# Kernel tuning notes

Measured on AMD Instinct MI355X. Metric: run time of the kernel, lower is better.

The kernel has to match this reference:

```python
import jax, jax.numpy as jnp
import numpy as np

H, W = 16, 16
DIM = 512
HEADS = 8
DIM_HEAD = 64
INNER = HEADS * DIM_HEAD  # 512
B = 8
N = H * W  # 256
SCALE = DIM_HEAD ** -0.5
EPS = 1e-5


def _index_map(h, w):
    # index_map[n, m] = dx * (2w-1) + dy with dx = x-i+h-1, dy = y-j+w-1
    xs = np.arange(h)
    ys = np.arange(w)
    dx = xs[:, None] - xs[None, :] + h - 1            # (h, h)
    dy = ys[:, None] - ys[None, :] + w - 1            # (w, w)
    idx = dx[:, None, :, None] * (2 * w - 1) + dy[None, :, None, :]  # (h, w, h, w)
    return idx.reshape(h * w, h * w).astype(np.int32)


def setup_inputs() -> dict:
    key = jax.random.key(0)
    ks = jax.random.split(key, 5)
    x = jax.random.normal(ks[0], (B, N, DIM), dtype=jnp.float32)
    ln_g = jnp.ones((DIM,), jnp.float32)
    ln_b = jnp.zeros((DIM,), jnp.float32)
    w_qkv = jax.random.normal(ks[1], (DIM, 3 * INNER), jnp.float32) * 0.02
    unique_params = jax.random.normal(ks[2], ((2 * H - 1) * (2 * W - 1), INNER), jnp.float32) * 0.02
    w_out = jax.random.normal(ks[3], (INNER, DIM), jnp.float32) * 0.02
    b_out = jnp.zeros((DIM,), jnp.float32)
    idx_map = jnp.asarray(_index_map(H, W))  # (N, N) int32
    return {"x": x, "ln_g": ln_g, "ln_b": ln_b, "w_qkv": w_qkv,
            "unique_params": unique_params, "w_out": w_out, "b_out": b_out,
            "idx_map": idx_map}


def reference(x, ln_g, ln_b, w_qkv, unique_params, w_out, b_out, idx_map):
    b, n, _ = x.shape
    # LayerNorm
    mu = jnp.mean(x, axis=-1, keepdims=True)
    var = jnp.mean(jnp.square(x - mu), axis=-1, keepdims=True)
    xn = (x - mu) * jax.lax.rsqrt(var + EPS) * ln_g + ln_b
    # qkv projection (no bias)
    qkv = xn @ w_qkv                                  # (b, n, 3*inner)
    q, k, v = jnp.split(qkv, 3, axis=-1)
    q = q.reshape(b, n, HEADS, DIM_HEAD)
    k = k.reshape(b, n, HEADS, DIM_HEAD)
    v = v.reshape(b, n, HEADS, DIM_HEAD)
    # attention scores
    dots = jnp.einsum('bnhd,bmhd->bhnm', q, k) * SCALE
    attn = jax.nn.softmax(dots, axis=-1)              # (b, h, n, m)
    # relative-position table: (n, m, h, d)
    rpos = unique_params[idx_map].reshape(n, n, HEADS, DIM_HEAD)
    # out[b,h,n,d] = sum_m attn[b,h,n,m] * (v[b,m,h,d] + rpos[n,m,h,d])
    out = jnp.einsum('bhnm,bmhd->bnhd', attn, v) \
        + jnp.einsum('bhnm,nmhd->bnhd', attn, rpos)
    out = out.reshape(b, n, INNER)
    return out @ w_out + b_out
```

## Files before the change

### kernel.cpp

```cpp
#include <hip/hip_runtime.h>
#include <math.h>

#define NB 8
#define SEQ 256
#define DIMC 512
#define NHEAD 8
#define DHEAD 64
#define SCALEF 0.125f

typedef __attribute__((ext_vector_type(8))) short s16x8;
typedef __attribute__((ext_vector_type(4))) float f32x4;

typedef __attribute__((address_space(3))) unsigned int lds_u32_t;
typedef const __attribute__((address_space(1))) unsigned int g_u32_t;
static __device__ __forceinline__ void gl_lds16(const void* gsrc, void* ldst) {
  __builtin_amdgcn_global_load_lds((g_u32_t*)gsrc, (lds_u32_t*)ldst, 16, 0, 0);
}

static __device__ __forceinline__ unsigned short f2bf(float f) {
  union { float f; unsigned u; } c; c.f = f;
  unsigned r = c.u + 0x7FFF + ((c.u >> 16) & 1);
  return (unsigned short)(r >> 16);
}
static __device__ __forceinline__ float bf2f(unsigned short u) {
  union { unsigned u; float f; } c; c.u = ((unsigned)u) << 16;
  return c.f;
}

static __device__ void tcast_body(const float* __restrict__ W,
    unsigned short* __restrict__ WT, int K, int N, int n0, int k0, int t,
    float (*tile)[65]) {
#pragma unroll
  for (int i = 0; i < 16; ++i) {
    const int idx = i * 256 + t;
    const int kl = idx >> 6, nl = idx & 63;
    tile[kl][nl] = W[(size_t)(k0 + kl) * N + n0 + nl];
  }
  __syncthreads();
#pragma unroll
  for (int i = 0; i < 16; ++i) {
    const int idx = i * 256 + t;
    const int nl = idx >> 6, kl = idx & 63;
    WT[(size_t)(n0 + nl) * K + k0 + kl] = f2bf(tile[kl][nl]);
  }
}

__global__ __launch_bounds__(256) void prep_kernel(const float* __restrict__ x,
    const float* __restrict__ g, const float* __restrict__ bta,
    const float* __restrict__ w_qkv, const float* __restrict__ w_out,
    const float* __restrict__ up, unsigned short* __restrict__ xnb,
    unsigned short* __restrict__ wqt, unsigned short* __restrict__ wot,
    unsigned short* __restrict__ upb) {
  __shared__ float tile[64][65];
  __shared__ float sh_s[4], sh_q[4];
  const int t = threadIdx.x;
  const int bid = blockIdx.x;
  if (bid < 192) {
    tcast_body(w_qkv, wqt, 512, 1536, (bid % 24) * 64, (bid / 24) * 64, t, tile);
  } else if (bid < 256) {
    const int b2 = bid - 192;
    tcast_body(w_out, wot, 512, 512, (b2 % 8) * 64, (b2 / 8) * 64, t, tile);
  } else if (bid < 497) {
    const int base = (bid - 256) * 2048 + t * 4;
#pragma unroll
    for (int it = 0; it < 2; ++it) {
      const int i = base + it * 1024;
      if (i < 492032) {
        const float4 v = *(const float4*)&up[i];
        ushort4 w;
        w.x = f2bf(v.x); w.y = f2bf(v.y); w.z = f2bf(v.z); w.w = f2bf(v.w);
        *(ushort4*)&upb[i] = w;
      }
    }
  } else {
    const int row = bid - 497;
    const float2 v = ((const float2*)(x + (size_t)row * DIMC))[t];
    float s = v.x + v.y;
    float q = v.x * v.x + v.y * v.y;
#pragma unroll
    for (int off = 32; off > 0; off >>= 1) {
      s += __shfl_down(s, off);
      q += __shfl_down(q, off);
    }
    const int wave = t >> 6, lane = t & 63;
    if (lane == 0) { sh_s[wave] = s; sh_q[wave] = q; }
    __syncthreads();
    const float fs = sh_s[0] + sh_s[1] + sh_s[2] + sh_s[3];
    const float fq = sh_q[0] + sh_q[1] + sh_q[2] + sh_q[3];
    const float mean = fs * (1.0f / DIMC);
    const float inv = rsqrtf(fq * (1.0f / DIMC) - mean * mean + 1e-5f);
    const float2 gv = ((const float2*)g)[t];
    const float2 bv = ((const float2*)bta)[t];
    ushort2 o;
    o.x = f2bf((v.x - mean) * inv * gv.x + bv.x);
    o.y = f2bf((v.y - mean) * inv * gv.y + bv.y);
    ((ushort2*)(xnb + (size_t)row * DIMC))[t] = o;
  }
}

template <int BM, int BN, bool BIAS, bool OUTBF, bool VSPLIT>
__global__ __launch_bounds__(256) void mfma_gemm_bt(
    const unsigned short* __restrict__ A, const unsigned short* __restrict__ BT,
    const float* __restrict__ bias, void* __restrict__ Cv,
    unsigned short* __restrict__ vtb, int M, int K, int N) {
  constexpr int TR = BM / 32;
  constexpr int TC = BN / 32;
  __shared__ unsigned short As[BM * 32];
  __shared__ unsigned short Bs[BN * 32];
  const int t = threadIdx.x;
  const int wave = t >> 6, lane = t & 63;
  const int wr = wave >> 1, wc = wave & 1;
  const int bm = blockIdx.x * BM, bn = blockIdx.y * BN;

  f32x4 acc[TR][TC] = {};

  const int fr = lane & 15, q4 = lane >> 4;
  const int kBlocks = K >> 5;
  for (int kb = 0; kb < kBlocks; ++kb) {
    const int k0 = kb << 5;
    __syncthreads();
#pragma unroll
    for (int c = 0; c < (BM * 4 + 255) / 256; ++c) {
      const int p = c * 256 + t;
      if (BM * 4 % 256 == 0 || p < BM * 4) {
        const int row = p >> 2;
        const int jl = (p & 3) ^ ((row >> 1) & 3);
        gl_lds16(A + (size_t)(bm + row) * K + k0 + jl * 8,
                 As + (size_t)(c * 256 + wave * 64) * 8);
      }
    }
#pragma unroll
    for (int c = 0; c < (BN * 4 + 255) / 256; ++c) {
      const int p = c * 256 + t;
      if (BN * 4 % 256 == 0 || p < BN * 4) {
        const int row = p >> 2;
        const int jl = (p & 3) ^ ((row >> 1) & 3);
        gl_lds16(BT + (size_t)(bn + row) * K + k0 + jl * 8,
                 Bs + (size_t)(c * 256 + wave * 64) * 8);
      }
    }
    __syncthreads();
    s16x8 af[TR], bfr[TC];
#pragma unroll
    for (int i = 0; i < TR; ++i) {
      const int row = wr * (BM / 2) + i * 16 + fr;
      const int jp = q4 ^ ((row >> 1) & 3);
      af[i] = *(const s16x8*)(As + row * 32 + jp * 8);
    }
#pragma unroll
    for (int j = 0; j < TC; ++j) {
      const int row = wc * (BN / 2) + j * 16 + fr;
      const int jp = q4 ^ ((row >> 1) & 3);
      bfr[j] = *(const s16x8*)(Bs + row * 32 + jp * 8);
    }
#pragma unroll
    for (int i = 0; i < TR; ++i)
#pragma unroll
      for (int j = 0; j < TC; ++j)
        acc[i][j] = __builtin_amdgcn_mfma_f32_16x16x32_bf16(af[i], bfr[j],
                                                            acc[i][j], 0, 0, 0);
  }
  if (VSPLIT && bn >= 1024) {
#pragma unroll
    for (int i = 0; i < TR; ++i) {
#pragma unroll
      for (int j = 0; j < TC; ++j) {
        const int hc = bn - 1024 + wc * (BN / 2) + j * 16 + fr;
        const int h = hc >> 6, d = hc & 63;
#pragma unroll
        for (int r = 0; r < 4; ++r) {
          const int row = bm + wr * (BM / 2) + i * 16 + q4 * 4 + r;
          const int b = row >> 8, m = row & 255;
          vtb[(size_t)((b * 8 + h) * 64 + d) * 256 + m] = f2bf(acc[i][j][r]);
        }
      }
    }
    return;
  }
#pragma unroll
  for (int i = 0; i < TR; ++i) {
#pragma unroll
    for (int j = 0; j < TC; ++j) {
      const int col = bn + wc * (BN / 2) + j * 16 + fr;
      const float bv = BIAS ? bias[col] : 0.0f;
#pragma unroll
      for (int r = 0; r < 4; ++r) {
        const int row = bm + wr * (BM / 2) + i * 16 + q4 * 4 + r;
        if constexpr (OUTBF) {
          ((unsigned short*)Cv)[(size_t)row * N + col] = f2bf(acc[i][j][r] + bv);
        } else {
          ((float*)Cv)[(size_t)row * N + col] = acc[i][j][r] + bv;
        }
      }
    }
  }
}

#define PSTR 264
#define KSTR 72
__global__ __launch_bounds__(128) void fused_attn_kernel(
    const unsigned short* __restrict__ qkvb, const unsigned short* __restrict__ vtb,
    unsigned short* __restrict__ attnb, unsigned short* __restrict__ oav) {
  __shared__ unsigned short kv_lds[256 * KSTR];
  __shared__ unsigned short p_lds[32 * PSTR];
  const int bh = blockIdx.y, b = bh >> 3, h = bh & 7;
  const int n0 = blockIdx.x * 32;
  const int t = threadIdx.x, wave = t >> 6, lane = t & 63;
  const int fr = lane & 15, q4 = lane >> 4;

#pragma unroll
  for (int p = 0; p < 16; ++p) {
    const int chunk = p * 128 + t;
    const int m = chunk >> 3, c = chunk & 7;
    *(s16x8*)(kv_lds + m * KSTR + c * 8) =
        *(const s16x8*)(qkvb + (size_t)(b * SEQ + m) * 1536 + 512 + h * 64 + c * 8);
  }
  s16x8 qf[2];
  {
    const size_t qrow = (size_t)(b * SEQ + n0 + wave * 16 + fr) * 1536 + h * 64;
#pragma unroll
    for (int ks = 0; ks < 2; ++ks)
      qf[ks] = *(const s16x8*)(qkvb + qrow + ks * 32 + q4 * 8);
  }
  __syncthreads();

  f32x4 s[16];
#pragma unroll
  for (int mt = 0; mt < 16; ++mt) s[mt] = (f32x4){0.f, 0.f, 0.f, 0.f};
#pragma unroll
  for (int ks = 0; ks < 2; ++ks)
#pragma unroll
    for (int mt = 0; mt < 16; ++mt) {
      const s16x8 kf =
          *(const s16x8*)(kv_lds + (mt * 16 + fr) * KSTR + ks * 32 + q4 * 8);
      s[mt] = __builtin_amdgcn_mfma_f32_16x16x32_bf16(qf[ks], kf, s[mt], 0, 0, 0);
    }

  float mx[4] = {-1e30f, -1e30f, -1e30f, -1e30f};
#pragma unroll
  for (int mt = 0; mt < 16; ++mt)
#pragma unroll
    for (int r = 0; r < 4; ++r) {
      s[mt][r] *= SCALEF;
      mx[r] = fmaxf(mx[r], s[mt][r]);
    }
#pragma unroll
  for (int r = 0; r < 4; ++r) {
    mx[r] = fmaxf(mx[r], __shfl_xor(mx[r], 1));
    mx[r] = fmaxf(mx[r], __shfl_xor(mx[r], 2));
    mx[r] = fmaxf(mx[r], __shfl_xor(mx[r], 4));
    mx[r] = fmaxf(mx[r], __shfl_xor(mx[r], 8));
  }
  float sum[4] = {0.f, 0.f, 0.f, 0.f};
#pragma unroll
  for (int mt = 0; mt < 16; ++mt)
#pragma unroll
    for (int r = 0; r < 4; ++r) {
      s[mt][r] = __expf(s[mt][r] - mx[r]);
      sum[r] += s[mt][r];
    }
#pragma unroll
  for (int r = 0; r < 4; ++r) {
    sum[r] += __shfl_xor(sum[r], 1);
    sum[r] += __shfl_xor(sum[r], 2);
    sum[r] += __shfl_xor(sum[r], 4);
    sum[r] += __shfl_xor(sum[r], 8);
  }
  const float invs[4] = {1.0f / sum[0], 1.0f / sum[1], 1.0f / sum[2],
                         1.0f / sum[3]};

  __syncthreads();

  {
    const int nb = wave * 16 + q4 * 4;
#pragma unroll
    for (int mt = 0; mt < 16; ++mt)
#pragma unroll
      for (int r = 0; r < 4; ++r)
        p_lds[(nb + r) * PSTR + mt * 16 + fr] = f2bf(s[mt][r] * invs[r]);
  }
#pragma unroll
  for (int p = 0; p < 16; ++p) {
    const int idx = p * 128 + t;
    const int d = idx >> 5, c = idx & 31;
    *(s16x8*)(kv_lds + d * PSTR + c * 8) =
        *(const s16x8*)(vtb + (size_t)(bh * 64 + d) * 256 + c * 8);
  }
  __syncthreads();

#pragma unroll
  for (int p = 0; p < 8; ++p) {
    const int idx = p * 128 + t;
    const int row = idx >> 5, mc = (idx & 31) * 8;
    *(s16x8*)(attnb + (size_t)(bh * SEQ + n0 + row) * SEQ + mc) =
        *(const s16x8*)(p_lds + row * PSTR + mc);
  }

  f32x4 o[4];
#pragma unroll
  for (int dt = 0; dt < 4; ++dt) o[dt] = (f32x4){0.f, 0.f, 0.f, 0.f};
#pragma unroll
  for (int ks = 0; ks < 8; ++ks) {
    const s16x8 pf =
        *(const s16x8*)(p_lds + (wave * 16 + fr) * PSTR + ks * 32 + q4 * 8);
#pragma unroll
    for (int dt = 0; dt < 4; ++dt) {
      const s16x8 vf =
          *(const s16x8*)(kv_lds + (dt * 16 + fr) * PSTR + ks * 32 + q4 * 8);
      o[dt] = __builtin_amdgcn_mfma_f32_16x16x32_bf16(pf, vf, o[dt], 0, 0, 0);
    }
  }
#pragma unroll
  for (int dt = 0; dt < 4; ++dt)
#pragma unroll
    for (int r = 0; r < 4; ++r) {
      const int n = n0 + wave * 16 + q4 * 4 + r;
      oav[(size_t)(b * SEQ + n) * DIMC + h * 64 + dt * 16 + fr] = f2bf(o[dt][r]);
    }
}

#define USTR 264
#define ASTR2 264
__global__ __launch_bounds__(256) void rpos_kernel(
    const unsigned short* __restrict__ attnb, const unsigned short* __restrict__ upb,
    unsigned short* __restrict__ ob) {
  __shared__ unsigned short upT[64 * USTR];
  __shared__ unsigned short aS[16 * ASTR2];
  const int t = threadIdx.x, wave = t >> 6, lane = t & 63;
  const int fr = lane & 15, q4 = lane >> 4;
  const int task = blockIdx.x;
  const int n = task >> 3, h = task & 7;
  const int xn = n >> 4, yn = n & 15;

  {
    const int b = t >> 5, mc = (t & 31) * 8;
    *(s16x8*)(aS + b * ASTR2 + mc) =
        *(const s16x8*)(attnb + (size_t)((b * 8 + h) * SEQ + n) * SEQ + mc);
  }
#pragma unroll
  for (int i = 0; i < 8; ++i) {
    const int chunk = i * 256 + t;
    const int m = chunk >> 3;
    const int g8 = chunk & 7;
    const int xm = m >> 4, ym = m & 15;
    const int row = (xn - xm + 15) * 31 + (yn - ym + 15);
    const s16x8 v = *(const s16x8*)(upb + (size_t)row * DIMC + h * 64 + g8 * 8);
    const int mc_phys = ((m >> 3) ^ g8) * 8 + (m & 7);
#pragma unroll
    for (int j = 0; j < 8; ++j)
      upT[(g8 * 8 + j) * USTR + mc_phys] = (unsigned short)v[j];
  }
  __syncthreads();

  f32x4 acc = (f32x4){0.f, 0.f, 0.f, 0.f};
  const int d = wave * 16 + fr;
#pragma unroll
  for (int ks = 0; ks < 8; ++ks) {
    const s16x8 af = *(const s16x8*)(aS + fr * ASTR2 + ks * 32 + q4 * 8);
    const int c_phys = (ks * 4 + q4) ^ (d >> 3);
    const s16x8 bf = *(const s16x8*)(upT + d * USTR + c_phys * 8);
    acc = __builtin_amdgcn_mfma_f32_16x16x32_bf16(af, bf, acc, 0, 0, 0);
  }
  if (q4 < 2) {
#pragma unroll
    for (int r = 0; r < 4; ++r) {
      const int b = q4 * 4 + r;
      unsigned short* p = ob + (size_t)(b * SEQ + n) * DIMC + h * 64 + d;
      *p = f2bf(bf2f(*p) + acc[r]);
    }
  }
}

extern "C" void kernel_launch(void* const* d_in, const int* in_sizes, int n_in,
                              void* d_out, int out_size, void* d_ws,
                              size_t ws_size, hipStream_t stream) {
  const float* x = (const float*)d_in[0];
  const float* ln_g = (const float*)d_in[1];
  const float* ln_b = (const float*)d_in[2];
  const float* w_qkv = (const float*)d_in[3];
  const float* up = (const float*)d_in[4];
  const float* w_out = (const float*)d_in[5];
  const float* b_out = (const float*)d_in[6];
  float* out = (float*)d_out;

  unsigned short* u = (unsigned short*)d_ws;
  unsigned short* qkvb = u;
  unsigned short* attnb = u + 3145728;
  unsigned short* xnb = u + 7340032;
  unsigned short* ob = u + 8388608;
  unsigned short* wqt = u + 9437184;
  unsigned short* wot = u + 10223616;
  unsigned short* upb = u + 10485760;
  unsigned short* vtb = u + 10977792;
  if (ws_size < (size_t)12026368 * sizeof(unsigned short)) return;

  prep_kernel<<<2545, 256, 0, stream>>>(x, ln_g, ln_b, w_qkv, w_out, up,
                                        xnb, wqt, wot, upb);
  mfma_gemm_bt<64, 64, false, true, true>
      <<<dim3(32, 24), 256, 0, stream>>>(xnb, wqt, nullptr, qkvb, vtb,
                                         2048, 512, 1536);
  fused_attn_kernel<<<dim3(8, 64), 128, 0, stream>>>(qkvb, vtb, attnb, ob);
  rpos_kernel<<<2048, 256, 0, stream>>>(attnb, upb, ob);
  mfma_gemm_bt<64, 32, true, false, false>
      <<<dim3(32, 16), 256, 0, stream>>>(ob, wot, b_out, out, nullptr,
                                         2048, 512, 512);
}
```

Measured before the change: 114.1 us.

## Fuse relative-position term into attention via scattered-probability GEMM against transposed table

Removes the separate rpos kernel and the global attention-probability buffer. Each attention block scatters its softmax probabilities into a zero-padded shared buffer indexed by relative-offset row, then does an MFMA GEMM against a transposed bf16 copy of the unique parameter table over a 544-wide window. K and V fragments are now read straight from global memory instead of being staged in LDS. The prep kernel now writes the parameter table transposed. This saves a launch and the read-modify-write round trip through global memory, at the cost of more MFMA work per block and uncoalesced global fragment loads.

```diff
diff --git a/kernel.cpp b/kernel.cpp
--- a/kernel.cpp
+++ b/kernel.cpp
@@ -22,10 +22,6 @@
   unsigned r = c.u + 0x7FFF + ((c.u >> 16) & 1);
   return (unsigned short)(r >> 16);
 }
-static __device__ __forceinline__ float bf2f(unsigned short u) {
-  union { unsigned u; float f; } c; c.u = ((unsigned)u) << 16;
-  return c.f;
-}
 
 static __device__ void tcast_body(const float* __restrict__ W,
     unsigned short* __restrict__ WT, int K, int N, int n0, int k0, int t,
@@ -50,7 +46,7 @@
     const float* __restrict__ w_qkv, const float* __restrict__ w_out,
     const float* __restrict__ up, unsigned short* __restrict__ xnb,
     unsigned short* __restrict__ wqt, unsigned short* __restrict__ wot,
-    unsigned short* __restrict__ upb) {
+    unsigned short* __restrict__ upT) {
   __shared__ float tile[64][65];
   __shared__ float sh_s[4], sh_q[4];
   const int t = threadIdx.x;
@@ -60,20 +56,26 @@
   } else if (bid < 256) {
     const int b2 = bid - 192;
     tcast_body(w_out, wot, 512, 512, (b2 % 8) * 64, (b2 / 8) * 64, t, tile);
-  } else if (bid < 497) {
-    const int base = (bid - 256) * 2048 + t * 4;
-#pragma unroll
-    for (int it = 0; it < 2; ++it) {
-      const int i = base + it * 1024;
-      if (i < 492032) {
-        const float4 v = *(const float4*)&up[i];
-        ushort4 w;
-        w.x = f2bf(v.x); w.y = f2bf(v.y); w.z = f2bf(v.z); w.w = f2bf(v.w);
-        *(ushort4*)&upb[i] = w;
-      }
+  } else if (bid < 384) {
+    const int b2 = bid - 256;
+    const int k0 = (b2 >> 3) * 64, n0 = (b2 & 7) * 64;
+#pragma unroll
+    for (int i = 0; i < 16; ++i) {
+      const int idx = i * 256 + t;
+      const int kl = idx >> 6, nl = idx & 63;
+      const int k = k0 + kl;
+      tile[kl][nl] = (k < 961) ? up[(size_t)k * 512 + n0 + nl] : 0.0f;
+    }
+    __syncthreads();
+#pragma unroll
+    for (int i = 0; i < 16; ++i) {
+      const int idx = i * 256 + t;
+      const int nl = idx >> 6, kl = idx & 63;
+      if (k0 + kl < 992)
+        upT[(size_t)(n0 + nl) * 992 + k0 + kl] = f2bf(tile[kl][nl]);
     }
   } else {
-    const int row = bid - 497;
+    const int row = bid - 384;
     const float2 v = ((const float2*)(x + (size_t)row * DIMC))[t];
     float s = v.x + v.y;
     float q = v.x * v.x + v.y * v.y;
@@ -197,24 +199,29 @@
 }
 
 #define PSTR 264
-#define KSTR 72
-__global__ __launch_bounds__(128) void fused_attn_kernel(
-    const unsigned short* __restrict__ qkvb, const unsigned short* __restrict__ vtb,
-    unsigned short* __restrict__ attnb, unsigned short* __restrict__ oav) {
-  __shared__ unsigned short kv_lds[256 * KSTR];
+#define ASTR 552
+__global__ __launch_bounds__(128) void attn_rpos_kernel(
+    const unsigned short* __restrict__ qkvb,
+    const unsigned short* __restrict__ vtb,
+    const unsigned short* __restrict__ upT,
+    unsigned short* __restrict__ ob) {
+  __shared__ unsigned short ascat[32 * ASTR];
   __shared__ unsigned short p_lds[32 * PSTR];
   const int bh = blockIdx.y, b = bh >> 3, h = bh & 7;
   const int n0 = blockIdx.x * 32;
   const int t = threadIdx.x, wave = t >> 6, lane = t & 63;
   const int fr = lane & 15, q4 = lane >> 4;
-
-#pragma unroll
-  for (int p = 0; p < 16; ++p) {
-    const int chunk = p * 128 + t;
-    const int m = chunk >> 3, c = chunk & 7;
-    *(s16x8*)(kv_lds + m * KSTR + c * 8) =
-        *(const s16x8*)(qkvb + (size_t)(b * SEQ + m) * 1536 + 512 + h * 64 + c * 8);
-  }
+  const int kwin0 = ((n0 >> 4) * 31) & ~7;
+
+  {
+    const s16x8 z = {0, 0, 0, 0, 0, 0, 0, 0};
+#pragma unroll
+    for (int i = 0; i < 18; ++i) {
+      const int idx = i * 128 + t;
+      if (idx < 32 * ASTR / 8) *(s16x8*)(ascat + idx * 8) = z;
+    }
+  }
+
   s16x8 qf[2];
   {
     const size_t qrow = (size_t)(b * SEQ + n0 + wave * 16 + fr) * 1536 + h * 64;
@@ -222,19 +229,21 @@
     for (int ks = 0; ks < 2; ++ks)
       qf[ks] = *(const s16x8*)(qkvb + qrow + ks * 32 + q4 * 8);
   }
-  __syncthreads();
 
   f32x4 s[16];
 #pragma unroll
   for (int mt = 0; mt < 16; ++mt) s[mt] = (f32x4){0.f, 0.f, 0.f, 0.f};
-#pragma unroll
-  for (int ks = 0; ks < 2; ++ks)
-#pragma unroll
-    for (int mt = 0; mt < 16; ++mt) {
-      const s16x8 kf =
-          *(const s16x8*)(kv_lds + (mt * 16 + fr) * KSTR + ks * 32 + q4 * 8);
-      s[mt] = __builtin_amdgcn_mfma_f32_16x16x32_bf16(qf[ks], kf, s[mt], 0, 0, 0);
-    }
+  {
+    const unsigned short* kb = qkvb + (size_t)(b * SEQ + fr) * 1536 + 512 + h * 64;
+#pragma unroll
+    for (int ks = 0; ks < 2; ++ks)
+#pragma unroll
+      for (int mt = 0; mt < 16; ++mt) {
+        const s16x8 kf =
+            *(const s16x8*)(kb + (size_t)mt * (16 * 1536) + ks * 32 + q4 * 8);
+        s[mt] = __builtin_amdgcn_mfma_f32_16x16x32_bf16(qf[ks], kf, s[mt], 0, 0, 0);
+      }
+  }
 
   float mx[4] = {-1e30f, -1e30f, -1e30f, -1e30f};
 #pragma unroll
@@ -271,43 +280,53 @@
 
   __syncthreads();
 
-  {
-    const int nb = wave * 16 + q4 * 4;
-#pragma unroll
-    for (int mt = 0; mt < 16; ++mt)
-#pragma unroll
-      for (int r = 0; r < 4; ++r)
-        p_lds[(nb + r) * PSTR + mt * 16 + fr] = f2bf(s[mt][r] * invs[r]);
-  }
-#pragma unroll
-  for (int p = 0; p < 16; ++p) {
-    const int idx = p * 128 + t;
-    const int d = idx >> 5, c = idx & 31;
-    *(s16x8*)(kv_lds + d * PSTR + c * 8) =
-        *(const s16x8*)(vtb + (size_t)(bh * 64 + d) * 256 + c * 8);
+  const int nb = wave * 16 + q4 * 4;
+#pragma unroll
+  for (int r = 0; r < 4; ++r) {
+    const int n = n0 + nb + r;
+    const int xn = n >> 4, yn = n & 15;
+    const int cb = (xn + 15) * 31 + (yn - fr + 15) - kwin0;
+    unsigned short* arow = ascat + (nb + r) * ASTR + cb;
+    unsigned short* prow = p_lds + (nb + r) * PSTR + fr;
+#pragma unroll
+    for (int mt = 0; mt < 16; ++mt) {
+      const unsigned short pb = f2bf(s[mt][r] * invs[r]);
+      prow[mt * 16] = pb;
+      arow[-(mt * 31)] = pb;
+    }
   }
   __syncthreads();
 
-#pragma unroll
-  for (int p = 0; p < 8; ++p) {
-    const int idx = p * 128 + t;
-    const int row = idx >> 5, mc = (idx & 31) * 8;
-    *(s16x8*)(attnb + (size_t)(bh * SEQ + n0 + row) * SEQ + mc) =
-        *(const s16x8*)(p_lds + row * PSTR + mc);
-  }
-
   f32x4 o[4];
 #pragma unroll
   for (int dt = 0; dt < 4; ++dt) o[dt] = (f32x4){0.f, 0.f, 0.f, 0.f};
-#pragma unroll
-  for (int ks = 0; ks < 8; ++ks) {
-    const s16x8 pf =
-        *(const s16x8*)(p_lds + (wave * 16 + fr) * PSTR + ks * 32 + q4 * 8);
-#pragma unroll
-    for (int dt = 0; dt < 4; ++dt) {
-      const s16x8 vf =
-          *(const s16x8*)(kv_lds + (dt * 16 + fr) * PSTR + ks * 32 + q4 * 8);
-      o[dt] = __builtin_amdgcn_mfma_f32_16x16x32_bf16(pf, vf, o[dt], 0, 0, 0);
+
+  {
+    const unsigned short* uB = upT + (size_t)(h * 64 + fr) * 992 + kwin0;
+    const unsigned short* aR = ascat + (wave * 16 + fr) * ASTR;
+#pragma unroll
+    for (int ks = 0; ks < 17; ++ks) {
+      const s16x8 af = *(const s16x8*)(aR + ks * 32 + q4 * 8);
+#pragma unroll
+      for (int dt = 0; dt < 4; ++dt) {
+        const s16x8 bfg =
+            *(const s16x8*)(uB + (size_t)dt * (16 * 992) + ks * 32 + q4 * 8);
+        o[dt] = __builtin_amdgcn_mfma_f32_16x16x32_bf16(af, bfg, o[dt], 0, 0, 0);
+      }
+    }
+  }
+  {
+    const unsigned short* vB = vtb + (size_t)(bh * 64 + fr) * 256;
+    const unsigned short* pR = p_lds + (wave * 16 + fr) * PSTR;
+#pragma unroll
+    for (int ks = 0; ks < 8; ++ks) {
+      const s16x8 pf = *(const s16x8*)(pR + ks * 32 + q4 * 8);
+#pragma unroll
+      for (int dt = 0; dt < 4; ++dt) {
+        const s16x8 vfg =
+            *(const s16x8*)(vB + (size_t)dt * (16 * 256) + ks * 32 + q4 * 8);
+        o[dt] = __builtin_amdgcn_mfma_f32_16x16x32_bf16(pf, vfg, o[dt], 0, 0, 0);
+      }
     }
   }
 #pragma unroll
@@ -315,60 +334,8 @@
 #pragma unroll
     for (int r = 0; r < 4; ++r) {
       const int n = n0 + wave * 16 + q4 * 4 + r;
-      oav[(size_t)(b * SEQ + n) * DIMC + h * 64 + dt * 16 + fr] = f2bf(o[dt][r]);
-    }
-}
-
-#define USTR 264
-#define ASTR2 264
-__global__ __launch_bounds__(256) void rpos_kernel(
-    const unsigned short* __restrict__ attnb, const unsigned short* __restrict__ upb,
-    unsigned short* __restrict__ ob) {
-  __shared__ unsigned short upT[64 * USTR];
-  __shared__ unsigned short aS[16 * ASTR2];
-  const int t = threadIdx.x, wave = t >> 6, lane = t & 63;
-  const int fr = lane & 15, q4 = lane >> 4;
-  const int task = blockIdx.x;
-  const int n = task >> 3, h = task & 7;
-  const int xn = n >> 4, yn = n & 15;
-
-  {
-    const int b = t >> 5, mc = (t & 31) * 8;
-    *(s16x8*)(aS + b * ASTR2 + mc) =
-        *(const s16x8*)(attnb + (size_t)((b * 8 + h) * SEQ + n) * SEQ + mc);
-  }
-#pragma unroll
-  for (int i = 0; i < 8; ++i) {
-    const int chunk = i * 256 + t;
-    const int m = chunk >> 3;
-    const int g8 = chunk & 7;
-    const int xm = m >> 4, ym = m & 15;
-    const int row = (xn - xm + 15) * 31 + (yn - ym + 15);
-    const s16x8 v = *(const s16x8*)(upb + (size_t)row * DIMC + h * 64 + g8 * 8);
-    const int mc_phys = ((m >> 3) ^ g8) * 8 + (m & 7);
-#pragma unroll
-    for (int j = 0; j < 8; ++j)
-      upT[(g8 * 8 + j) * USTR + mc_phys] = (unsigned short)v[j];
-  }
-  __syncthreads();
-
-  f32x4 acc = (f32x4){0.f, 0.f, 0.f, 0.f};
-  const int d = wave * 16 + fr;
-#pragma unroll
-  for (int ks = 0; ks < 8; ++ks) {
-    const s16x8 af = *(const s16x8*)(aS + fr * ASTR2 + ks * 32 + q4 * 8);
-    const int c_phys = (ks * 4 + q4) ^ (d >> 3);
-    const s16x8 bf = *(const s16x8*)(upT + d * USTR + c_phys * 8);
-    acc = __builtin_amdgcn_mfma_f32_16x16x32_bf16(af, bf, acc, 0, 0, 0);
-  }
-  if (q4 < 2) {
-#pragma unroll
-    for (int r = 0; r < 4; ++r) {
-      const int b = q4 * 4 + r;
-      unsigned short* p = ob + (size_t)(b * SEQ + n) * DIMC + h * 64 + d;
-      *p = f2bf(bf2f(*p) + acc[r]);
-    }
-  }
+      ob[(size_t)(b * SEQ + n) * DIMC + h * 64 + dt * 16 + fr] = f2bf(o[dt][r]);
+    }
 }
 
 extern "C" void kernel_launch(void* const* d_in, const int* in_sizes, int n_in,
@@ -385,22 +352,20 @@
 
   unsigned short* u = (unsigned short*)d_ws;
   unsigned short* qkvb = u;
-  unsigned short* attnb = u + 3145728;
-  unsigned short* xnb = u + 7340032;
-  unsigned short* ob = u + 8388608;
-  unsigned short* wqt = u + 9437184;
-  unsigned short* wot = u + 10223616;
-  unsigned short* upb = u + 10485760;
-  unsigned short* vtb = u + 10977792;
-  if (ws_size < (size_t)12026368 * sizeof(unsigned short)) return;
-
-  prep_kernel<<<2545, 256, 0, stream>>>(x, ln_g, ln_b, w_qkv, w_out, up,
-                                        xnb, wqt, wot, upb);
+  unsigned short* xnb = u + 3145728;
+  unsigned short* ob = u + 4194304;
+  unsigned short* wqt = u + 5242880;
+  unsigned short* wot = u + 6029312;
+  unsigned short* upT = u + 6291456;
+  unsigned short* vtb = u + 6799360;
+  if (ws_size < (size_t)7847936 * sizeof(unsigned short)) return;
+
+  prep_kernel<<<2432, 256, 0, stream>>>(x, ln_g, ln_b, w_qkv, w_out, up,
+                                        xnb, wqt, wot, upT);
   mfma_gemm_bt<64, 64, false, true, true>
       <<<dim3(32, 24), 256, 0, stream>>>(xnb, wqt, nullptr, qkvb, vtb,
                                          2048, 512, 1536);
-  fused_attn_kernel<<<dim3(8, 64), 128, 0, stream>>>(qkvb, vtb, attnb, ob);
-  rpos_kernel<<<2048, 256, 0, stream>>>(attnb, upb, ob);
+  attn_rpos_kernel<<<dim3(8, 64), 128, 0, stream>>>(qkvb, vtb, upT, ob);
   mfma_gemm_bt<64, 32, true, false, false>
       <<<dim3(32, 16), 256, 0, stream>>>(ob, wot, b_out, out, nullptr,
                                          2048, 512, 512);
```

After: 118.3 us. 1.04x slower.
